# Kernel tuning notes

Measured on AMD Instinct MI355X. Metric: run time of the kernel, lower is better.

## Reference

```python
import jax, jax.numpy as jnp
import numpy as np

B, L, C, H, Wd = 256, 64, 256, 32, 32  # batch, num_filts, code_dim, height, width

def setup_inputs() -> dict:
    key = jax.random.key(0)
    k1, k2 = jax.random.split(key)
    code = jax.random.normal(k1, (B, L, C), dtype=jnp.float32)
    # stacked per-filter weights: weights[l].weight has shape [code_dim, H*W]
    W = jax.random.normal(k2, (L, C, H * Wd), dtype=jnp.float32) * (1.0 / np.sqrt(C))
    return {"code": code, "W": W}

def reference(code, W):
    # Original: for each filter l, x_hat[:, l] = code[:, l, :] @ weights[l].weight
    # (F.linear(x, weight.t()) == x @ weight). Fuse into one batched GEMM.
    # code: [B, L, C], W: [L, C, HW] -> out: [B, L, HW]
    x_hat = jnp.einsum('blc,lcd->bld', code, W)
    return x_hat.reshape(code.shape[0], W.shape[0], H, Wd)
```

## Files before the change

### kernel.cpp

```cpp
#include <hip/hip_runtime.h>
#include <hip/hip_bf16.h>

#define B_  256
#define L_  64
#define C_  256
#define HW_ 1024

typedef float  floatx4 __attribute__((ext_vector_type(4)));
typedef __bf16 bf16x8  __attribute__((ext_vector_type(8)));
typedef __bf16 bf16x4  __attribute__((ext_vector_type(4)));

#define LDT 72

#define BARRIER_LDS() asm volatile("s_waitcnt lgkmcnt(0)\n\ts_barrier" ::: "memory")

__global__ __launch_bounds__(512, 4)
void gld_mfma_kernel(const float* __restrict__ code,
                     const float* __restrict__ W,
                     float* __restrict__ out)
{
    const int tid = threadIdx.x;
    const int l   = blockIdx.z;
    const int m0  = blockIdx.y * 128;
    const int n0  = blockIdx.x * 128;

    __shared__ __bf16 Alds[128 * LDT];
    __shared__ __bf16 Blds[128 * LDT];

    const int lane = tid & 63;
    const int wave = tid >> 6;
    const int wm = (wave >> 2) * 64;
    const int wn = (wave & 3) * 32;

    floatx4 acc[4][2];
    #pragma unroll
    for (int i = 0; i < 4; ++i)
        #pragma unroll
        for (int j = 0; j < 2; ++j)
            acc[i][j] = (floatx4)0.0f;

    const int a_row = tid >> 4;
    const int a_kc  = (tid & 15) * 4;
    const int b_i  = tid & 31;
    const int b_g  = tid >> 5;
    const int b_kq = (b_g + b_i) & 15;

    const float* aBase = code + (size_t)m0 * (L_ * C_) + (size_t)l * C_ + a_kc;
    const float* wBase = W + (size_t)l * (C_ * HW_) + n0 + 4 * b_i;

    floatx4 Areg[4];
    floatx4 Breg[2][4];

    #pragma unroll
    for (int p = 0; p < 4; ++p)
        Areg[p] = *(const floatx4*)(aBase + (size_t)(p * 32 + a_row) * (L_ * C_));
    #pragma unroll
    for (int r = 0; r < 4; ++r)
        Breg[0][r] = *(const floatx4*)(wBase + (size_t)(4 * b_kq + r) * HW_);
    #pragma unroll
    for (int r = 0; r < 4; ++r)
        Breg[1][r] = *(const floatx4*)(wBase + (size_t)(64 + 4 * b_kq + r) * HW_);

    #pragma unroll
    for (int kb = 0; kb < C_; kb += 64) {
        const int pb = (kb >> 6) & 1;

        #pragma unroll
        for (int j = 0; j < 4; ++j) {
            bf16x4 h;
            h.x = (__bf16)Breg[pb][0][j]; h.y = (__bf16)Breg[pb][1][j];
            h.z = (__bf16)Breg[pb][2][j]; h.w = (__bf16)Breg[pb][3][j];
            *(bf16x4*)&Blds[(4 * b_i + j) * LDT + 4 * b_kq] = h;
        }
        #pragma unroll
        for (int p = 0; p < 4; ++p) {
            bf16x4 h;
            h.x = (__bf16)Areg[p].x; h.y = (__bf16)Areg[p].y;
            h.z = (__bf16)Areg[p].z; h.w = (__bf16)Areg[p].w;
            *(bf16x4*)&Alds[(p * 32 + a_row) * LDT + a_kc] = h;
        }

        if (kb + 64 < C_) {
            #pragma unroll
            for (int p = 0; p < 4; ++p)
                Areg[p] = *(const floatx4*)(aBase + (size_t)(p * 32 + a_row) * (L_ * C_) + (kb + 64));
        }
        if (kb + 128 < C_) {
            #pragma unroll
            for (int r = 0; r < 4; ++r)
                Breg[pb][r] = *(const floatx4*)(wBase + (size_t)(kb + 128 + 4 * b_kq + r) * HW_);
        }

        BARRIER_LDS();

        #pragma unroll
        for (int ks = 0; ks < 2; ++ks) {
            bf16x8 af[4], bfr[2];
            const int koff = ks * 32 + (lane >> 4) * 8;
            #pragma unroll
            for (int i = 0; i < 4; ++i)
                af[i] = *(const bf16x8*)&Alds[(wm + i * 16 + (lane & 15)) * LDT + koff];
            #pragma unroll
            for (int j = 0; j < 2; ++j)
                bfr[j] = *(const bf16x8*)&Blds[(wn + j * 16 + (lane & 15)) * LDT + koff];
            #pragma unroll
            for (int i = 0; i < 4; ++i)
                #pragma unroll
                for (int j = 0; j < 2; ++j)
                    acc[i][j] = __builtin_amdgcn_mfma_f32_16x16x32_bf16(af[i], bfr[j], acc[i][j], 0, 0, 0);
        }

        BARRIER_LDS();
    }

    const int col0 = lane & 15;
    const int row0 = (lane >> 4) * 4;
    #pragma unroll
    for (int i = 0; i < 4; ++i) {
        #pragma unroll
        for (int j = 0; j < 2; ++j) {
            const int m = m0 + wm + i * 16 + row0;
            const int n = n0 + wn + j * 16 + col0;
            float* o = out + (size_t)m * (L_ * HW_) + (size_t)l * HW_ + n;
            #pragma unroll
            for (int r = 0; r < 4; ++r)
                o[(size_t)r * (L_ * HW_)] = acc[i][j][r];
        }
    }
}

extern "C" void kernel_launch(void* const* d_in, const int* in_sizes, int n_in,
                              void* d_out, int out_size, void* d_ws, size_t ws_size,
                              hipStream_t stream) {
    const float* code = (const float*)d_in[0];
    const float* W    = (const float*)d_in[1];
    float* out        = (float*)d_out;

    dim3 grid(HW_ / 128, B_ / 128, L_);
    gld_mfma_kernel<<<grid, 512, 0, stream>>>(code, W, out);
}
```

Before: 149.0 us.

## Double-buffer A prefetch and remap B LDS stores with row rotation

The A-tile global loads now use a two-stage register double buffer, as B already did, so loads are issued two K-steps ahead. The B global load pattern drops the diagonal k-quad skew, so each thread group reads contiguous k rows. LDS conflicts are instead avoided by rotating rows within groups of four, and a matching rot_row mapping is applied on the read side. This raises register use, which may affect occupancy under the 512x4 launch bounds, in exchange for hiding more load latency.

```diff
diff --git a/kernel.cpp b/kernel.cpp
--- a/kernel.cpp
+++ b/kernel.cpp
@@ -13,6 +13,10 @@
 #define LDT 72
 
 #define BARRIER_LDS() asm volatile("s_waitcnt lgkmcnt(0)\n\ts_barrier" ::: "memory")
+
+__device__ __forceinline__ int rot_row(int n) {
+    return (n & ~3) | ((n + (n >> 2)) & 3);
+}
 
 __global__ __launch_bounds__(512, 4)
 void gld_mfma_kernel(const float* __restrict__ code,
@@ -42,53 +46,54 @@
     const int a_row = tid >> 4;
     const int a_kc  = (tid & 15) * 4;
     const int b_i  = tid & 31;
-    const int b_g  = tid >> 5;
-    const int b_kq = (b_g + b_i) & 15;
+    const int b_kt = (tid >> 5) * 4;
 
     const float* aBase = code + (size_t)m0 * (L_ * C_) + (size_t)l * C_ + a_kc;
-    const float* wBase = W + (size_t)l * (C_ * HW_) + n0 + 4 * b_i;
+    const float* wBase = W + (size_t)l * (C_ * HW_) + (size_t)b_kt * HW_ + n0 + 4 * b_i;
 
-    floatx4 Areg[4];
+    floatx4 Areg[2][4];
     floatx4 Breg[2][4];
 
     #pragma unroll
     for (int p = 0; p < 4; ++p)
-        Areg[p] = *(const floatx4*)(aBase + (size_t)(p * 32 + a_row) * (L_ * C_));
+        Areg[0][p] = *(const floatx4*)(aBase + (size_t)(p * 32 + a_row) * (L_ * C_));
+    #pragma unroll
+    for (int p = 0; p < 4; ++p)
+        Areg[1][p] = *(const floatx4*)(aBase + (size_t)(p * 32 + a_row) * (L_ * C_) + 64);
     #pragma unroll
     for (int r = 0; r < 4; ++r)
-        Breg[0][r] = *(const floatx4*)(wBase + (size_t)(4 * b_kq + r) * HW_);
+        Breg[0][r] = *(const floatx4*)(wBase + (size_t)r * HW_);
     #pragma unroll
     for (int r = 0; r < 4; ++r)
-        Breg[1][r] = *(const floatx4*)(wBase + (size_t)(64 + 4 * b_kq + r) * HW_);
+        Breg[1][r] = *(const floatx4*)(wBase + (size_t)(64 + r) * HW_);
 
     #pragma unroll
     for (int kb = 0; kb < C_; kb += 64) {
         const int pb = (kb >> 6) & 1;
 
         #pragma unroll
+        for (int p = 0; p < 4; ++p) {
+            bf16x4 h;
+            h.x = (__bf16)Areg[pb][p].x; h.y = (__bf16)Areg[pb][p].y;
+            h.z = (__bf16)Areg[pb][p].z; h.w = (__bf16)Areg[pb][p].w;
+            *(bf16x4*)&Alds[(p * 32 + a_row) * LDT + a_kc] = h;
+        }
+        #pragma unroll
         for (int j = 0; j < 4; ++j) {
             bf16x4 h;
             h.x = (__bf16)Breg[pb][0][j]; h.y = (__bf16)Breg[pb][1][j];
             h.z = (__bf16)Breg[pb][2][j]; h.w = (__bf16)Breg[pb][3][j];
-            *(bf16x4*)&Blds[(4 * b_i + j) * LDT + 4 * b_kq] = h;
-        }
-        #pragma unroll
-        for (int p = 0; p < 4; ++p) {
-            bf16x4 h;
-            h.x = (__bf16)Areg[p].x; h.y = (__bf16)Areg[p].y;
-            h.z = (__bf16)Areg[p].z; h.w = (__bf16)Areg[p].w;
-            *(bf16x4*)&Alds[(p * 32 + a_row) * LDT + a_kc] = h;
+            const int prow = 4 * b_i + ((j + b_i) & 3);
+            *(bf16x4*)&Blds[prow * LDT + b_kt] = h;
         }
 
-        if (kb + 64 < C_) {
+        if (kb + 128 < C_) {
             #pragma unroll
             for (int p = 0; p < 4; ++p)
-                Areg[p] = *(const floatx4*)(aBase + (size_t)(p * 32 + a_row) * (L_ * C_) + (kb + 64));
-        }
-        if (kb + 128 < C_) {
+                Areg[pb][p] = *(const floatx4*)(aBase + (size_t)(p * 32 + a_row) * (L_ * C_) + (kb + 128));
             #pragma unroll
             for (int r = 0; r < 4; ++r)
-                Breg[pb][r] = *(const floatx4*)(wBase + (size_t)(kb + 128 + 4 * b_kq + r) * HW_);
+                Breg[pb][r] = *(const floatx4*)(wBase + (size_t)(kb + 128 + r) * HW_);
         }
 
         BARRIER_LDS();
@@ -101,8 +106,10 @@
             for (int i = 0; i < 4; ++i)
                 af[i] = *(const bf16x8*)&Alds[(wm + i * 16 + (lane & 15)) * LDT + koff];
             #pragma unroll
-            for (int j = 0; j < 2; ++j)
-                bfr[j] = *(const bf16x8*)&Blds[(wn + j * 16 + (lane & 15)) * LDT + koff];
+            for (int j = 0; j < 2; ++j) {
+                const int n = wn + j * 16 + (lane & 15);
+                bfr[j] = *(const bf16x8*)&Blds[rot_row(n) * LDT + koff];
+            }
             #pragma unroll
             for (int i = 0; i < 4; ++i)
                 #pragma unroll
```

After: 145.9 us. 2.1% less time.

## Swizzle B LDS layout, coalesce W loads, and remap block order

Applied to the files above, without the earlier changes.

Replaces the rotated k-quad B staging (padded rows) with an XOR-swizzled 128-byte-row LDS layout, so each thread loads a contiguous 4-row strip of W instead of a rotated one. Global W reads become more uniform, and bank conflicts on the transposed B stores and bf16x8 reads are meant to shrink. The launch also becomes a 1D grid that interleaves 8 filters per group, which changes the block scheduling order for L2 and XCD locality. The risk is extra address arithmetic and a possible loss of write conflict avoidance.

```diff
diff --git a/kernel.cpp b/kernel.cpp
--- a/kernel.cpp
+++ b/kernel.cpp
@@ -10,9 +10,12 @@
 typedef __bf16 bf16x8  __attribute__((ext_vector_type(8)));
 typedef __bf16 bf16x4  __attribute__((ext_vector_type(4)));
 
-#define LDT 72
+#define LDT_A 72
+#define LDB_ROW 128
 
 #define BARRIER_LDS() asm volatile("s_waitcnt lgkmcnt(0)\n\ts_barrier" ::: "memory")
+
+__device__ __forceinline__ int bswz(int n) { return (n ^ (n >> 2)) & 7; }
 
 __global__ __launch_bounds__(512, 4)
 void gld_mfma_kernel(const float* __restrict__ code,
@@ -20,12 +23,16 @@
                      float* __restrict__ out)
 {
     const int tid = threadIdx.x;
-    const int l   = blockIdx.z;
-    const int m0  = blockIdx.y * 128;
-    const int n0  = blockIdx.x * 128;
 
-    __shared__ __bf16 Alds[128 * LDT];
-    __shared__ __bf16 Blds[128 * LDT];
+    const int id  = blockIdx.x;
+    const int ll  = id & 7;
+    const int inr = id >> 3;
+    const int m0  = (inr & 1) * 128;
+    const int n0  = ((inr >> 1) & 7) * 128;
+    const int l   = (inr >> 4) * 8 + ll;
+
+    __shared__ __bf16 Alds[128 * LDT_A];
+    __shared__ unsigned char Blds[128 * LDB_ROW];
 
     const int lane = tid & 63;
     const int wave = tid >> 6;
@@ -42,11 +49,10 @@
     const int a_row = tid >> 4;
     const int a_kc  = (tid & 15) * 4;
     const int b_i  = tid & 31;
-    const int b_g  = tid >> 5;
-    const int b_kq = (b_g + b_i) & 15;
+    const int b_c8 = tid >> 5;
 
     const float* aBase = code + (size_t)m0 * (L_ * C_) + (size_t)l * C_ + a_kc;
-    const float* wBase = W + (size_t)l * (C_ * HW_) + n0 + 4 * b_i;
+    const float* wBase = W + (size_t)l * (C_ * HW_) + (size_t)(4 * b_c8) * HW_ + n0 + 4 * b_i;
 
     floatx4 Areg[4];
     floatx4 Breg[2][4];
@@ -56,10 +62,17 @@
         Areg[p] = *(const floatx4*)(aBase + (size_t)(p * 32 + a_row) * (L_ * C_));
     #pragma unroll
     for (int r = 0; r < 4; ++r)
-        Breg[0][r] = *(const floatx4*)(wBase + (size_t)(4 * b_kq + r) * HW_);
+        Breg[0][r] = *(const floatx4*)(wBase + (size_t)r * HW_);
     #pragma unroll
     for (int r = 0; r < 4; ++r)
-        Breg[1][r] = *(const floatx4*)(wBase + (size_t)(64 + 4 * b_kq + r) * HW_);
+        Breg[1][r] = *(const floatx4*)(wBase + (size_t)(64 + r) * HW_);
+
+    int bwaddr[4];
+    #pragma unroll
+    for (int j = 0; j < 4; ++j) {
+        const int row = 4 * b_i + j;
+        bwaddr[j] = row * LDB_ROW + (((b_c8 >> 1) ^ bswz(row)) << 4) + ((b_c8 & 1) << 3);
+    }
 
     #pragma unroll
     for (int kb = 0; kb < C_; kb += 64) {
@@ -70,14 +83,14 @@
             bf16x4 h;
             h.x = (__bf16)Breg[pb][0][j]; h.y = (__bf16)Breg[pb][1][j];
             h.z = (__bf16)Breg[pb][2][j]; h.w = (__bf16)Breg[pb][3][j];
-            *(bf16x4*)&Blds[(4 * b_i + j) * LDT + 4 * b_kq] = h;
+            *(bf16x4*)&Blds[bwaddr[j]] = h;
         }
         #pragma unroll
         for (int p = 0; p < 4; ++p) {
             bf16x4 h;
             h.x = (__bf16)Areg[p].x; h.y = (__bf16)Areg[p].y;
             h.z = (__bf16)Areg[p].z; h.w = (__bf16)Areg[p].w;
-            *(bf16x4*)&Alds[(p * 32 + a_row) * LDT + a_kc] = h;
+            *(bf16x4*)&Alds[(p * 32 + a_row) * LDT_A + a_kc] = h;
         }
 
         if (kb + 64 < C_) {
@@ -88,7 +101,7 @@
         if (kb + 128 < C_) {
             #pragma unroll
             for (int r = 0; r < 4; ++r)
-                Breg[pb][r] = *(const floatx4*)(wBase + (size_t)(kb + 128 + 4 * b_kq + r) * HW_);
+                Breg[pb][r] = *(const floatx4*)(wBase + (size_t)(kb + 128 + r) * HW_);
         }
 
         BARRIER_LDS();
@@ -99,10 +112,12 @@
             const int koff = ks * 32 + (lane >> 4) * 8;
             #pragma unroll
             for (int i = 0; i < 4; ++i)
-                af[i] = *(const bf16x8*)&Alds[(wm + i * 16 + (lane & 15)) * LDT + koff];
+                af[i] = *(const bf16x8*)&Alds[(wm + i * 16 + (lane & 15)) * LDT_A + koff];
             #pragma unroll
-            for (int j = 0; j < 2; ++j)
-                bfr[j] = *(const bf16x8*)&Blds[(wn + j * 16 + (lane & 15)) * LDT + koff];
+            for (int j = 0; j < 2; ++j) {
+                const int n = wn + j * 16 + (lane & 15);
+                bfr[j] = *(const bf16x8*)&Blds[n * LDB_ROW + (((koff >> 3) ^ bswz(n)) << 4)];
+            }
             #pragma unroll
             for (int i = 0; i < 4; ++i)
                 #pragma unroll
@@ -136,6 +151,5 @@
     const float* W    = (const float*)d_in[1];
     float* out        = (float*)d_out;
 
-    dim3 grid(HW_ / 128, B_ / 128, L_);
-    gld_mfma_kernel<<<grid, 512, 0, stream>>>(code, W, out);
+    gld_mfma_kernel<<<dim3(1024), 512, 0, stream>>>(code, W, out);
 }
```

Result: faster. 132.1 us (-11.3%).
